# Kernel optimization log

Hardware: AMD Instinct MI355X
Metric: run time of the kernel (lower is better)

The kernel has to match this reference:

```python
import jax, jax.numpy as jnp
import numpy as np

N_EXAMPLES = 32768
N_CLASSES = 1000
N_BINS = 15


def setup_inputs() -> dict:
    key = jax.random.key(0)
    k1, k2 = jax.random.split(key)
    # logits as produced by the (frozen) base model
    logits = jax.random.normal(k1, (N_EXAMPLES, N_CLASSES), dtype=jnp.float32) * 3.0
    # per-bin accuracy estimates from histogram_binning(); -1.0 marks an empty bin
    histogram = jax.random.uniform(k2, (N_BINS,), dtype=jnp.float32)
    histogram = histogram.at[0].set(-1.0)
    return {"logits": logits, "histogram": histogram}


def reference(logits, histogram):
    """Vectorized histogram-binning calibration.

    Returns (sm_calib [N,C], valid_flag [N], predictions [N]) matching
    forward() -> get_calibrated_softmax_vector() of the torch module.
    """
    n_bins = histogram.shape[0]
    n_classes = logits.shape[1]

    sm = jax.nn.softmax(logits, axis=1)                      # [N, C]
    conf = jnp.max(sm, axis=1)                               # argmax softmax score
    pred = jnp.argmax(sm, axis=1)                            # [N]

    # torch.histc bins are (lower, upper]; index = ceil(conf * n_bins) - 1
    bin_idx = jnp.clip(jnp.ceil(conf * n_bins).astype(jnp.int32) - 1, 0, n_bins - 1)
    h = histogram[bin_idx]                                   # [N] bin accuracy lookup
    valid_flag = (h != -1.0).astype(jnp.float32)
    # empty bin (-1) -> fall back to raw confidence
    est = jnp.where(h == -1.0, conf, h)                      # [N]

    onehot = jax.nn.one_hot(pred, n_classes, dtype=sm.dtype)  # [N, C]
    masked = sm * (1.0 - onehot)                              # zero out argmax entry
    denom = jnp.sum(masked, axis=1, keepdims=True)            # mass of the rest
    rescaled = (1.0 - est)[:, None] * masked / denom
    rescaled = rescaled * (1.0 - onehot) + est[:, None] * onehot
    # final renormalization (sums to 1 up to fp error, kept for faithfulness)
    sm_calib = rescaled / jnp.sum(rescaled, axis=1, keepdims=True)
    return sm_calib, valid_flag, pred
```

## Files before the change

kernel.cpp:

```cpp
#include <hip/hip_runtime.h>
#include <math.h>


constexpr int N_EX    = 32768;
constexpr int N_CLS   = 1000;
constexpr int N_BINS  = 15;
constexpr int C4      = N_CLS / 4;

__global__ __launch_bounds__(256) void hb_calib_kernel(
    const float* __restrict__ logits,
    const float* __restrict__ hist,
    float* __restrict__ out)
{
    const int wave = threadIdx.x >> 6;
    const int lane = threadIdx.x & 63;
    const int row  = blockIdx.x * 4 + wave;
    if (row >= N_EX) return;

    const float4* lrow = reinterpret_cast<const float4*>(logits + (size_t)row * N_CLS);

    float4 v[4];
    float lmax = -INFINITY;
    int   lidx = N_CLS;
    #pragma unroll
    for (int r = 0; r < 4; ++r) {
        const int q = lane + 64 * r;
        if (q < C4) {
            v[r] = lrow[q];
            float* f = reinterpret_cast<float*>(&v[r]);
            #pragma unroll
            for (int t = 0; t < 4; ++t) {
                const int col = 4 * q + t;
                const float x = f[t];
                if (x > lmax) { lmax = x; lidx = col; }
            }
        }
    }

    float m   = lmax;
    int   mix = lidx;
    #pragma unroll
    for (int off = 32; off >= 1; off >>= 1) {
        const float ov = __shfl_xor(m, off);
        const int   oi = __shfl_xor(mix, off);
        if (ov > m || (ov == m && oi < mix)) { m = ov; mix = oi; }
    }

    float lsum = 0.0f;
    #pragma unroll
    for (int r = 0; r < 4; ++r) {
        const int q = lane + 64 * r;
        if (q < C4) {
            float* f = reinterpret_cast<float*>(&v[r]);
            #pragma unroll
            for (int t = 0; t < 4; ++t) {
                const int col = 4 * q + t;
                const float e = __expf(f[t] - m);
                f[t] = e;
                if (col != mix) lsum += e;
            }
        }
    }
    float srest = lsum;
    #pragma unroll
    for (int off = 32; off >= 1; off >>= 1) srest += __shfl_xor(srest, off);

    const float s    = srest + 1.0f;
    const float conf = 1.0f / s;

    int bin = (int)ceilf(conf * (float)N_BINS) - 1;
    bin = bin < 0 ? 0 : (bin > N_BINS - 1 ? N_BINS - 1 : bin);
    const float h     = hist[bin];
    const float valid = (h != -1.0f) ? 1.0f : 0.0f;
    const float est   = (h == -1.0f) ? conf : h;

    const float scale = (1.0f - est) / srest;

    float4* orow = reinterpret_cast<float4*>(out + (size_t)row * N_CLS);
    #pragma unroll
    for (int r = 0; r < 4; ++r) {
        const int q = lane + 64 * r;
        if (q < C4) {
            float* f = reinterpret_cast<float*>(&v[r]);
            float4 o;
            float* of = reinterpret_cast<float*>(&o);
            #pragma unroll
            for (int t = 0; t < 4; ++t) {
                const int col = 4 * q + t;
                of[t] = (col == mix) ? est : f[t] * scale;
            }
            orow[q] = o;
        }
    }

    if (lane == 0) {
        const size_t base = (size_t)N_EX * N_CLS;
        out[base + row]        = valid;
        out[base + N_EX + row] = (float)mix;
    }
}

extern "C" void kernel_launch(void* const* d_in, const int* in_sizes, int n_in,
                              void* d_out, int out_size, void* d_ws, size_t ws_size,
                              hipStream_t stream) {
    const float* logits = (const float*)d_in[0];
    const float* hist   = (const float*)d_in[1];
    float* out          = (float*)d_out;

    const int rows_per_block = 4;
    const int grid = (N_EX + rows_per_block - 1) / rows_per_block;
    hb_calib_kernel<<<grid, 256, 0, stream>>>(logits, hist, out);
}
```

Before: 46.54 us.

## Hoist unconditional row loads, use nontemporal stores, simplify exp sum

All four vector loads per lane are now issued up front and unconditionally, with the index clamped, so they are all in flight before the max reduction. The intent is more memory-level parallelism. Output stores use nontemporal hints so the large write stream does not pollute the cache. The exponential sum now includes the argmax term and subtracts 1 afterwards, which drops a per-element compare but slightly changes floating-point rounding of the rest-mass.

```diff
diff --git a/kernel.cpp b/kernel.cpp
--- a/kernel.cpp
+++ b/kernel.cpp
@@ -7,6 +7,8 @@
 constexpr int N_BINS  = 15;
 constexpr int C4      = N_CLS / 4;
 
+typedef float vf4 __attribute__((ext_vector_type(4)));
+
 __global__ __launch_bounds__(256) void hb_calib_kernel(
     const float* __restrict__ logits,
     const float* __restrict__ hist,
@@ -15,23 +17,27 @@
     const int wave = threadIdx.x >> 6;
     const int lane = threadIdx.x & 63;
     const int row  = blockIdx.x * 4 + wave;
-    if (row >= N_EX) return;
 
-    const float4* lrow = reinterpret_cast<const float4*>(logits + (size_t)row * N_CLS);
+    const vf4* lrow = reinterpret_cast<const vf4*>(logits + (size_t)row * N_CLS);
 
-    float4 v[4];
+    vf4 v[4];
+    #pragma unroll
+    for (int r = 0; r < 4; ++r) {
+        const int q  = lane + 64 * r;
+        const int ql = (q < C4) ? q : (C4 - 1);
+        v[r] = lrow[ql];
+    }
+
     float lmax = -INFINITY;
     int   lidx = N_CLS;
     #pragma unroll
     for (int r = 0; r < 4; ++r) {
         const int q = lane + 64 * r;
         if (q < C4) {
-            v[r] = lrow[q];
-            float* f = reinterpret_cast<float*>(&v[r]);
             #pragma unroll
             for (int t = 0; t < 4; ++t) {
                 const int col = 4 * q + t;
-                const float x = f[t];
+                const float x = v[r][t];
                 if (x > lmax) { lmax = x; lidx = col; }
             }
         }
@@ -51,22 +57,20 @@
     for (int r = 0; r < 4; ++r) {
         const int q = lane + 64 * r;
         if (q < C4) {
-            float* f = reinterpret_cast<float*>(&v[r]);
             #pragma unroll
             for (int t = 0; t < 4; ++t) {
-                const int col = 4 * q + t;
-                const float e = __expf(f[t] - m);
-                f[t] = e;
-                if (col != mix) lsum += e;
+                const float e = __expf(v[r][t] - m);
+                v[r][t] = e;
+                lsum += e;
             }
         }
     }
-    float srest = lsum;
+    float s = lsum;
     #pragma unroll
-    for (int off = 32; off >= 1; off >>= 1) srest += __shfl_xor(srest, off);
+    for (int off = 32; off >= 1; off >>= 1) s += __shfl_xor(s, off);
 
-    const float s    = srest + 1.0f;
-    const float conf = 1.0f / s;
+    const float srest = s - 1.0f;
+    const float conf  = 1.0f / s;
 
     int bin = (int)ceilf(conf * (float)N_BINS) - 1;
     bin = bin < 0 ? 0 : (bin > N_BINS - 1 ? N_BINS - 1 : bin);
@@ -76,27 +80,25 @@
 
     const float scale = (1.0f - est) / srest;
 
-    float4* orow = reinterpret_cast<float4*>(out + (size_t)row * N_CLS);
+    vf4* orow = reinterpret_cast<vf4*>(out + (size_t)row * N_CLS);
     #pragma unroll
     for (int r = 0; r < 4; ++r) {
         const int q = lane + 64 * r;
         if (q < C4) {
-            float* f = reinterpret_cast<float*>(&v[r]);
-            float4 o;
-            float* of = reinterpret_cast<float*>(&o);
+            vf4 o;
             #pragma unroll
             for (int t = 0; t < 4; ++t) {
                 const int col = 4 * q + t;
-                of[t] = (col == mix) ? est : f[t] * scale;
+                o[t] = (col == mix) ? est : v[r][t] * scale;
             }
-            orow[q] = o;
+            __builtin_nontemporal_store(o, &orow[q]);
         }
     }
 
     if (lane == 0) {
         const size_t base = (size_t)N_EX * N_CLS;
-        out[base + row]        = valid;
-        out[base + N_EX + row] = (float)mix;
+        __builtin_nontemporal_store(valid, &out[base + row]);
+        __builtin_nontemporal_store((float)mix, &out[base + N_EX + row]);
     }
 }
 
```

Result: faster. 44.52 us (-4.3%).
